# Kernel optimization log

Measured on AMD Instinct MI355X. Metric: run time of the kernel, lower is better.

## Reference

```python
import jax, jax.numpy as jnp
import numpy as np

NA, NT, E = 8000, 30000, 150000
H, C, HID = 4, 64, 64  # heads, per-head out_channels, hidden_dim
AF, TF = 32, 48


def _gat(x_src, x_dst, src, dst, W, a_src, a_dst, bias, n_dst):
    # PyG GATConv, concat=False, add_self_loops=False, eval (no dropout)
    h_src = (x_src @ W).reshape(-1, H, C)          # [Ns,H,C]
    h_dst = (x_dst @ W).reshape(-1, H, C)          # [Nd,H,C]
    al_s = jnp.sum(h_src * a_src, axis=-1)         # [Ns,H]
    al_d = jnp.sum(h_dst * a_dst, axis=-1)         # [Nd,H]
    e = jax.nn.leaky_relu(al_s[src] + al_d[dst], 0.2)  # [E,H]
    m = jax.ops.segment_max(e, dst, num_segments=n_dst)
    m = jnp.where(jnp.isfinite(m), m, 0.0)
    ex = jnp.exp(e - m[dst])
    den = jax.ops.segment_sum(ex, dst, num_segments=n_dst)
    alpha = ex / (den[dst] + 1e-16)                # per-dst softmax
    out = jax.ops.segment_sum(alpha[:, :, None] * h_src[src], dst, num_segments=n_dst)
    return jnp.mean(out, axis=1) + bias            # mean over heads + bias


def _bn(x, g, b):  # BatchNorm1d, training-mode batch stats, biased var
    mu = jnp.mean(x, axis=0)
    v = jnp.var(x, axis=0)
    return g * (x - mu) * jax.lax.rsqrt(v + 1e-5) + b


def _ln(x, g, b):
    mu = jnp.mean(x, axis=-1, keepdims=True)
    v = jnp.var(x, axis=-1, keepdims=True)
    return g * (x - mu) * jax.lax.rsqrt(v + 1e-5) + b


def setup_inputs() -> dict:
    key = jax.random.key(0)
    ks = jax.random.split(key, 40)
    n = lambda i, shp, s=0.05: jax.random.normal(ks[i], shp, jnp.float32) * s
    ri = lambda i, hi: jax.random.randint(ks[i], (E,), 0, hi, jnp.int32)
    inp = {
        'x_agent': jax.random.normal(ks[0], (NA, AF), jnp.float32),
        'x_track': jax.random.normal(ks[1], (NT, TF), jnp.float32),
        'ei_a2t1_src': ri(2, NA), 'ei_a2t1_dst': ri(3, NT),
        'ei_t2a1_src': ri(4, NT), 'ei_t2a1_dst': ri(5, NA),
        'ei_a2t2_src': ri(6, NA), 'ei_a2t2_dst': ri(7, NT),
        'ei_t2a2_src': ri(8, NT), 'ei_t2a2_dst': ri(9, NA),
        'ae_W': n(10, (AF, HID)), 'ae_b': jnp.zeros((HID,), jnp.float32),
        'te_W': n(11, (TF, HID)), 'te_b': jnp.zeros((HID,), jnp.float32),
        # stacked GATConv params: [layer=3, relation=4, ...]; rel order: a2t1,t2a1,a2t2,t2a2
        'conv_W': n(12, (3, 4, HID, H * C)),
        'conv_asrc': n(13, (3, 4, H, C)),
        'conv_adst': n(14, (3, 4, H, C)),
        'conv_bias': jnp.zeros((3, 4, C), jnp.float32),
        'bn_gamma': jnp.ones((3, 2, HID), jnp.float32),   # [layer, agent/track, HID]
        'bn_beta': jnp.zeros((3, 2, HID), jnp.float32),
        # actor heads: 0=agent_alpha,1=agent_beta,2=track_alpha,3=track_beta
        'actor_W1': n(15, (4, HID, HID // 2)), 'actor_b1': jnp.zeros((4, HID // 2), jnp.float32),
        'actor_g': jnp.ones((4, HID // 2), jnp.float32), 'actor_be': jnp.zeros((4, HID // 2), jnp.float32),
        'actor_W2': n(16, (4, HID // 2, 1)), 'actor_b2': jnp.zeros((4, 1), jnp.float32),
        # critic global value head
        'cW1': n(17, (HID * 6, HID * 2)), 'cb1': jnp.zeros((HID * 2,), jnp.float32),
        'cg1': jnp.ones((HID * 2,), jnp.float32), 'cbe1': jnp.zeros((HID * 2,), jnp.float32),
        'cW2': n(18, (HID * 2, HID)), 'cb2': jnp.zeros((HID,), jnp.float32),
        'cg2': jnp.ones((HID,), jnp.float32), 'cbe2': jnp.zeros((HID,), jnp.float32),
        'cW3': n(19, (HID, HID // 2)), 'cb3': jnp.zeros((HID // 2,), jnp.float32),
        'cW4': n(20, (HID // 2, 1)), 'cb4': jnp.zeros((1,), jnp.float32),
    }
    return inp


def _forward(x_agent, x_track,
             ei_a2t1_src, ei_a2t1_dst, ei_t2a1_src, ei_t2a1_dst,
             ei_a2t2_src, ei_a2t2_dst, ei_t2a2_src, ei_t2a2_dst,
             ae_W, ae_b, te_W, te_b,
             conv_W, conv_asrc, conv_adst, conv_bias,
             bn_gamma, bn_beta,
             actor_W1, actor_b1, actor_g, actor_be, actor_W2, actor_b2,
             cW1, cb1, cg1, cbe1, cW2, cb2, cg2, cbe2, cW3, cb3, cW4, cb4):
    xa = jax.nn.relu(x_agent @ ae_W + ae_b)
    xt = jax.nn.relu(x_track @ te_W + te_b)
    prev_a, prev_t = None, None
    for l in range(3):
        # HeteroConv aggr='mean': track <- mean(rel0, rel2); agent <- mean(rel1, rel3)
        ot = 0.5 * (_gat(xa, xt, ei_a2t1_src, ei_a2t1_dst, conv_W[l, 0], conv_asrc[l, 0], conv_adst[l, 0], conv_bias[l, 0], NT)
                    + _gat(xa, xt, ei_a2t2_src, ei_a2t2_dst, conv_W[l, 2], conv_asrc[l, 2], conv_adst[l, 2], conv_bias[l, 2], NT))
        oa = 0.5 * (_gat(xt, xa, ei_t2a1_src, ei_t2a1_dst, conv_W[l, 1], conv_asrc[l, 1], conv_adst[l, 1], conv_bias[l, 1], NA)
                    + _gat(xt, xa, ei_t2a2_src, ei_t2a2_dst, conv_W[l, 3], conv_asrc[l, 3], conv_adst[l, 3], conv_bias[l, 3], NA))
        oa = _bn(jax.nn.relu(oa), bn_gamma[l, 0], bn_beta[l, 0])
        ot = _bn(jax.nn.relu(ot), bn_gamma[l, 1], bn_beta[l, 1])
        if l > 0:  # residuals after layers 2 and 3
            oa = oa + prev_a
            ot = ot + prev_t
        prev_a, prev_t = oa, ot
        xa, xt = oa, ot

    def head(x, i):
        h = jax.nn.relu(_ln(x @ actor_W1[i] + actor_b1[i], actor_g[i], actor_be[i]))
        return jax.nn.softplus(h @ actor_W2[i] + actor_b2[i]) + 1.0

    aA, aB = head(xa, 0), head(xa, 1)
    tA, tB = head(xt, 2), head(xt, 3)
    aC = aA / (aA + aB)
    tC = tA / (tA + tB)

    # critic global value (torch.std is unbiased, ddof=1)
    g = jnp.concatenate([
        jnp.mean(xa, axis=0), jnp.max(xa, axis=0), jnp.std(xa, axis=0, ddof=1),
        jnp.mean(xt, axis=0), jnp.max(xt, axis=0), jnp.std(xt, axis=0, ddof=1)], axis=0)[None, :]
    h = jax.nn.relu(_ln(g @ cW1 + cb1, cg1, cbe1))
    h = jax.nn.relu(_ln(h @ cW2 + cb2, cg2, cbe2))
    h = jax.nn.relu(h @ cW3 + cb3)
    gv = jnp.squeeze(h @ cW4 + cb4)
    return aA, aB, aC, tA, tB, tC, gv


def reference(x_agent, x_track,
              ei_a2t1_src, ei_a2t1_dst, ei_t2a1_src, ei_t2a1_dst,
              ei_a2t2_src, ei_a2t2_dst, ei_t2a2_src, ei_t2a2_dst,
              ae_W, ae_b, te_W, te_b,
              conv_W, conv_asrc, conv_adst, conv_bias,
              bn_gamma, bn_beta,
              actor_W1, actor_b1, actor_g, actor_be, actor_W2, actor_b2,
              cW1, cb1, cg1, cbe1, cW2, cb2, cg2, cbe2, cW3, cb3, cW4, cb4):
    return _forward(x_agent, x_track,
                    ei_a2t1_src, ei_a2t1_dst, ei_t2a1_src, ei_t2a1_dst,
                    ei_a2t2_src, ei_a2t2_dst, ei_t2a2_src, ei_t2a2_dst,
                    ae_W, ae_b, te_W, te_b,
                    conv_W, conv_asrc, conv_adst, conv_bias,
                    bn_gamma, bn_beta,
                    actor_W1, actor_b1, actor_g, actor_be, actor_W2, actor_b2,
                    cW1, cb1, cg1, cbe1, cW2, cb2, cg2, cbe2, cW3, cb3, cW4, cb4)
```

## Files before the change

kernel.cpp:

```cpp
#include <hip/hip_runtime.h>
#include <math.h>

#define NAg 8000
#define NTr 30000
#define NE  150000

#define XA_OFF 0
#define XT_OFF 512000
#define H0_OFF 2432000
#define H1_OFF 4480000
#define H2_OFF 12160000
#define H3_OFF 14208000
#define BNSTB 8320000
#define ALS0 21888000
#define ALS1 21920000
#define ALS2 22040000
#define ALS3 22072000
#define ALD0 22192000
#define ALD1 22312000
#define ALD2 22344000
#define ALD3 22464000
#define ESRC_I 22496000
#define OAACC 23104000
#define OTACC 23616000
#define BNST 25536000
#define CST  25536256
#define ROWP_I 25536640
#define CURS_I 25656704
#define RELSTRIDE 30016

typedef unsigned short ushortT;

__device__ __forceinline__ float lrelu(float x){ return x >= 0.f ? x : 0.2f*x; }
__device__ __forceinline__ unsigned fmap(float f){ unsigned u=__float_as_uint(f); return (u&0x80000000u)? ~u : (u|0x80000000u); }
__device__ __forceinline__ float funmap(unsigned u){ return (u&0x80000000u)? __uint_as_float(u&0x7FFFFFFFu) : __uint_as_float(~u); }
__device__ __forceinline__ float softplusf(float x){ return fmaxf(x,0.f) + log1pf(expf(-fabsf(x))); }
__device__ __forceinline__ ushortT f2bf(float f){
  unsigned u = __float_as_uint(f);
  unsigned r = u + 0x7FFFu + ((u>>16)&1u);
  return (ushortT)(r>>16);
}
__device__ __forceinline__ float bf2f(ushortT s){ return __uint_as_float(((unsigned)s)<<16); }
__device__ __forceinline__ float wred32(float v){
  #pragma unroll
  for (int o=16;o;o>>=1) v += __shfl_xor(v,o,32);
  return v;
}
__device__ __forceinline__ int selH(int r){ return r==0?H0_OFF: r==1?H1_OFF: r==2?H2_OFF:H3_OFF; }
__device__ __forceinline__ int selALS(int r){ return r==0?ALS0: r==1?ALS1: r==2?ALS2:ALS3; }
__device__ __forceinline__ int selALD(int r){ return r==0?ALD0: r==1?ALD1: r==2?ALD2:ALD3; }

__global__ __launch_bounds__(256) void k_encoder(const float* xA, const float* xT,
    const float* aeW, const float* aeB, const float* teW, const float* teB, float* ws) {
  int type = blockIdx.y;
  int N = type ? NTr : NAg;
  int t = threadIdx.x, wv = t >> 6, lane = t & 63;
  int n = blockIdx.x*4 + wv;
  int F = type ? 48 : 32;
  const float* X = type ? xT : xA;
  const float* W = type ? teW : aeW;
  const float* B = type ? teB : aeB;
  float* out = ws + (type ? XT_OFF : XA_OFF);
  __shared__ float xs[4][48];
  if (n < N && lane < F) xs[wv][lane] = X[(size_t)n*F + lane];
  __syncthreads();
  if (n >= N) return;
  float acc = B[lane];
  for (int k = 0; k < F; ++k) acc += xs[wv][k] * W[k*64 + lane];
  out[(size_t)n*64 + lane] = fmaxf(acc, 0.f);
}

__global__ __launch_bounds__(256) void k_hist(const int* d0_,const int* d1_,const int* d2_,const int* d3_,
                                              int* wsi) {
  int r = blockIdx.y;
  const int* dp = r==0? d0_ : r==1? d1_ : r==2? d2_ : d3_;
  int e = blockIdx.x*256 + threadIdx.x;
  if (e >= NE) return;
  atomicAdd(&wsi[ROWP_I + r*RELSTRIDE + dp[e]], 1);
}

__global__ __launch_bounds__(256) void k_scan(int* wsi) {
  int r = blockIdx.x;
  int n = ((r & 1) ? NAg : NTr) + 1;
  int* rp = wsi + ROWP_I + r*RELSTRIDE;
  __shared__ int part[256];
  int t = threadIdx.x;
  int chunk = (n + 255) / 256;
  int lo = t*chunk, hi = min(lo + chunk, n);
  int s = 0;
  for (int i = lo; i < hi; ++i) s += rp[i];
  part[t] = s;
  __syncthreads();
  if (t == 0) {
    int run = 0;
    for (int i = 0; i < 256; ++i) { int tm = part[i]; part[i] = run; run += tm; }
  }
  __syncthreads();
  int run = part[t];
  for (int i = lo; i < hi; ++i) { int tm = rp[i]; rp[i] = run; run += tm; }
}

__global__ __launch_bounds__(256) void k_fill(const int* s0,const int* d0_,const int* s1,const int* d1_,
    const int* s2,const int* d2_,const int* s3,const int* d3_, int* wsi) {
  int r = blockIdx.y;
  const int* sp = r==0? s0 : r==1? s1 : r==2? s2 : s3;
  const int* dp = r==0? d0_ : r==1? d1_ : r==2? d2_ : d3_;
  int e = blockIdx.x*256 + threadIdx.x;
  if (e >= NE) return;
  int d = dp[e];
  int pos = wsi[ROWP_I + r*RELSTRIDE + d] + atomicAdd(&wsi[CURS_I + r*RELSTRIDE + d], 1);
  wsi[ESRC_I + r*NE + pos] = sp[e];
}

__global__ __launch_bounds__(256) void k_alx(const float* convW, const float* convAsrc,
                                             const float* convAdst, float* ws, int layer) {
  int y = blockIdx.y;
  int side = y >> 2;
  int r = y & 3;
  int Nn = side ? ((r & 1) ? NTr : NAg) : ((r & 1) ? NAg : NTr);
  if (blockIdx.x * 64 >= Nn) return;
  const float* W  = convW + (size_t)(layer*4 + r)*64*256;
  const float* av = (side ? convAsrc : convAdst) + (size_t)(layer*4 + r)*256;
  __shared__ float Wv[64*4];
  int t = threadIdx.x;
  {
    int k = t >> 2, h = t & 3;
    float s = 0.f;
    for (int c = 0; c < 64; ++c) s += W[k*256 + h*64 + c] * av[h*64 + c];
    Wv[k*4 + h] = s;
  }
  __syncthreads();
  const float* xv = ws + (side ? ((r & 1) ? XT_OFF : XA_OFF) : ((r & 1) ? XA_OFF : XT_OFF));
  float* outp = ws + (side ? selALS(r) : selALD(r));
  int n = blockIdx.x * 64 + (t >> 2);
  if (n >= Nn) return;
  int h = t & 3;
  float s = 0.f;
  for (int k = 0; k < 64; ++k) s += xv[(size_t)n*64 + k] * Wv[k*4 + h];
  outp[n*4 + h] = s;
}

__global__ __launch_bounds__(256) void k_hgemm(const float* convW, float* ws, int layer) {
  int tile = blockIdx.x;
  int r, row0;
  if (tile < 500)        { r = 0; row0 = tile*16; }
  else if (tile < 2375)  { r = 1; row0 = (tile-500)*16; }
  else if (tile < 2875)  { r = 2; row0 = (tile-2375)*16; }
  else                   { r = 3; row0 = (tile-2875)*16; }
  const float* W  = convW + (size_t)(layer*4 + r)*64*256;
  const float* xg = ws + ((r & 1) ? XT_OFF : XA_OFF);
  ushortT* h16 = (ushortT*)(ws + selH(r));
  __shared__ float xs[16][64];
  int t = threadIdx.x;
  #pragma unroll
  for (int i = 0; i < 4; ++i) {
    int lin = i*256 + t;
    xs[lin>>6][lin&63] = xg[((size_t)row0 + (lin>>6))*64 + (lin&63)];
  }
  __syncthreads();
  int c0 = t & 63;
  int tr = t >> 6;
  float acc[4][4];
  #pragma unroll
  for (int i=0;i<4;i++){ acc[i][0]=0;acc[i][1]=0;acc[i][2]=0;acc[i][3]=0; }
  const float* Wc = W + c0;
  for (int k4 = 0; k4 < 16; ++k4) {
    float4 xv[4];
    #pragma unroll
    for (int i = 0; i < 4; ++i) xv[i] = *(const float4*)&xs[tr*4+i][k4*4];
    #pragma unroll
    for (int kk = 0; kk < 4; ++kk) {
      int k = k4*4 + kk;
      float w0 = Wc[k*256], w1 = Wc[k*256+64], w2 = Wc[k*256+128], w3 = Wc[k*256+192];
      #pragma unroll
      for (int i = 0; i < 4; ++i) {
        float x = (kk==0)?xv[i].x:(kk==1)?xv[i].y:(kk==2)?xv[i].z:xv[i].w;
        acc[i][0] += x*w0; acc[i][1] += x*w1; acc[i][2] += x*w2; acc[i][3] += x*w3;
      }
    }
  }
  #pragma unroll
  for (int i = 0; i < 4; ++i) {
    int row = row0 + tr*4 + i;
    ushort4 pk;
    pk.x = f2bf(acc[i][0]); pk.y = f2bf(acc[i][1]);
    pk.z = f2bf(acc[i][2]); pk.w = f2bf(acc[i][3]);
    *(ushort4*)(h16 + (size_t)row*256 + c0*4) = pk;
  }
}

__global__ __launch_bounds__(256) void k_agg(const float* convBias, float* ws, int layer) {
  int type = blockIdx.y;
  int N = type ? NAg : NTr;
  if (blockIdx.x * 4 >= N) return;
  int t = threadIdx.x, lane = t & 63, hh = lane & 3, base = lane & ~3;
  int node = blockIdx.x*4 + (t >> 6);
  const int* wsi = (const int*)ws;
  float outv = 0.f;
  #pragma unroll
  for (int rr = 0; rr < 2; ++rr) {
    int r = type ? (rr ? 3 : 1) : (rr ? 2 : 0);
    const int* rp = wsi + ROWP_I + r*RELSTRIDE;
    const int* es = wsi + ESRC_I + r*NE;
    const float* als = ws + selALS(r);
    const ushortT* h16 = (const ushortT*)(ws + selH(r));
    float ad = (ws + selALD(r))[node*4 + hh];
    int p = rp[node], p1 = rp[node+1];
    float num0=0.f, num1=0.f, num2=0.f, num3=0.f, den=0.f;
    for (; p + 4 <= p1; p += 4) {
      int sa = es[p], sb = es[p+1], sc = es[p+2], sd4 = es[p+3];
      ushort4 va = *(const ushort4*)(h16 + (size_t)sa*256 + lane*4);
      ushort4 vb = *(const ushort4*)(h16 + (size_t)sb*256 + lane*4);
      ushort4 vc = *(const ushort4*)(h16 + (size_t)sc*256 + lane*4);
      ushort4 vd = *(const ushort4*)(h16 + (size_t)sd4*256 + lane*4);
      float la = als[sa*4+hh], lb = als[sb*4+hh], lc = als[sc*4+hh], ld = als[sd4*4+hh];
      float ea = __expf(lrelu(la + ad));
      float eb = __expf(lrelu(lb + ad));
      float ec = __expf(lrelu(lc + ad));
      float ed = __expf(lrelu(ld + ad));
      den += (ea+eb)+(ec+ed);
      float qa0=__shfl(ea,base), qa1=__shfl(ea,base+1), qa2=__shfl(ea,base+2), qa3=__shfl(ea,base+3);
      float qb0=__shfl(eb,base), qb1=__shfl(eb,base+1), qb2=__shfl(eb,base+2), qb3=__shfl(eb,base+3);
      float qc0=__shfl(ec,base), qc1=__shfl(ec,base+1), qc2=__shfl(ec,base+2), qc3=__shfl(ec,base+3);
      float qd0=__shfl(ed,base), qd1=__shfl(ed,base+1), qd2=__shfl(ed,base+2), qd3=__shfl(ed,base+3);
      num0 += qa0*bf2f(va.x) + qb0*bf2f(vb.x) + qc0*bf2f(vc.x) + qd0*bf2f(vd.x);
      num1 += qa1*bf2f(va.y) + qb1*bf2f(vb.y) + qc1*bf2f(vc.y) + qd1*bf2f(vd.y);
      num2 += qa2*bf2f(va.z) + qb2*bf2f(vb.z) + qc2*bf2f(vc.z) + qd2*bf2f(vd.z);
      num3 += qa3*bf2f(va.w) + qb3*bf2f(vb.w) + qc3*bf2f(vc.w) + qd3*bf2f(vd.w);
    }
    for (; p < p1; ++p) {
      int s = es[p];
      ushort4 va = *(const ushort4*)(h16 + (size_t)s*256 + lane*4);
      float e = __expf(lrelu(als[s*4 + hh] + ad));
      den += e;
      float q0 = __shfl(e, base), q1 = __shfl(e, base+1), q2 = __shfl(e, base+2), q3 = __shfl(e, base+3);
      num0 += q0*bf2f(va.x); num1 += q1*bf2f(va.y); num2 += q2*bf2f(va.z); num3 += q3*bf2f(va.w);
    }
    float rd = 1.f/(den + 1e-16f);
    float r0 = __shfl(rd, base), r1 = __shfl(rd, base+1), r2 = __shfl(rd, base+2), r3 = __shfl(rd, base+3);
    outv += num0*r0 + num1*r1 + num2*r2 + num3*r3;
  }
  int rA = type ? 1 : 0, rB = type ? 3 : 2;
  float bavg = 0.5f*(convBias[(layer*4 + rA)*64 + lane] + convBias[(layer*4 + rB)*64 + lane]);
  float z = fmaxf(outv*0.125f + bavg, 0.f);
  float* acc = ws + (type ? OAACC : OTACC);
  acc[(size_t)node*64 + lane] = z;
  __shared__ float sdm[2][256];
  sdm[0][t] = z; sdm[1][t] = z*z;
  __syncthreads();
  if (t < 64) {
    float s1 = sdm[0][t] + sdm[0][t+64] + sdm[0][t+128] + sdm[0][t+192];
    float s2 = sdm[1][t] + sdm[1][t+64] + sdm[1][t+128] + sdm[1][t+192];
    int bt = type ? 0 : 1;
    int bucket = blockIdx.x & 63;
    atomicAdd(&ws[BNSTB + bucket*256 + bt*128 + t], s1);
    atomicAdd(&ws[BNSTB + bucket*256 + bt*128 + 64 + t], s2);
  }
}

__global__ __launch_bounds__(256) void k_bnred(float* ws) {
  int t = threadIdx.x;
  float s = 0.f;
  #pragma unroll
  for (int b = 0; b < 64; ++b) s += ws[BNSTB + b*256 + t];
  ws[BNST + t] = s;
}

__global__ __launch_bounds__(256) void k_bnnorm(const float* bnG, const float* bnB, float* ws, int layer) {
  int type = blockIdx.y;
  int N = type ? NTr : NAg;
  float* acc = ws + (type ? OTACC : OAACC);
  float* x = ws + (type ? XT_OFF : XA_OFF);
  int i = blockIdx.x*256 + threadIdx.x;
  if (i >= N*64) return;
  int c = i & 63;
  float Nf = (float)N;
  float s1 = ws[BNST + type*128 + c], s2 = ws[BNST + type*128 + 64 + c];
  float mu = s1/Nf, var = s2/Nf - mu*mu;
  float g = bnG[(layer*2 + type)*64 + c], b = bnB[(layer*2 + type)*64 + c];
  float y = g*(acc[i]-mu)*rsqrtf(var + 1e-5f) + b;
  if (layer > 0) y += x[i];
  x[i] = y;
}

__global__ __launch_bounds__(256) void k_actor(const float* aW1, const float* ab1, const float* ag,
    const float* abe, const float* aW2, const float* ab2, const float* ws, float* out) {
  int type = blockIdx.y;
  int N = type ? NTr : NAg;
  int t = threadIdx.x, wv = t >> 6, lane = t & 63;
  int p = lane >> 5, j = lane & 31;
  int n = blockIdx.x*4 + wv;
  const float* xg = ws + (type ? XT_OFF : XA_OFF);
  __shared__ float xsh[4][64];
  {
    int nn = blockIdx.x*4 + (t >> 6);
    if (nn < N) xsh[t >> 6][t & 63] = xg[(size_t)nn*64 + (t & 63)];
  }
  __syncthreads();
  if (n >= N) return;
  int i = (type ? 2 : 0) + p;
  const float* W = aW1 + i*2048 + j;
  float a0 = 0.f, a1 = 0.f, a2 = 0.f, a3 = 0.f;
  #pragma unroll
  for (int k = 0; k < 64; k += 4) {
    a0 += xsh[wv][k]   * W[k*32];
    a1 += xsh[wv][k+1] * W[(k+1)*32];
    a2 += xsh[wv][k+2] * W[(k+2)*32];
    a3 += xsh[wv][k+3] * W[(k+3)*32];
  }
  float tv = ((a0+a1)+(a2+a3)) + ab1[i*32 + j];
  float mu = wred32(tv) * (1.f/32.f);
  float dz = tv - mu;
  float var = wred32(dz*dz) * (1.f/32.f);
  float hn = fmaxf(ag[i*32+j]*dz*rsqrtf(var + 1e-5f) + abe[i*32+j], 0.f);
  float s = wred32(hn * aW2[i*32 + j]) + ab2[i];
  float val = softplusf(s) + 1.f;
  float vA = __shfl(val, 0);
  float vB = __shfl(val, 32);
  if (lane == 0) {
    int offA = type ? 24000 : 0, offB = type ? 54000 : 8000, offC = type ? 84000 : 16000;
    out[offA + n] = vA;
    out[offB + n] = vB;
    out[offC + n] = vA / (vA + vB);
  }
}

__global__ __launch_bounds__(256) void k_criticstats(float* ws) {
  int type = blockIdx.y;
  int N = type ? NTr : NAg;
  const float* x = ws + (type ? XT_OFF : XA_OFF);
  int t = threadIdx.x;
  int c = t & 63;
  float s1 = 0.f, s2 = 0.f, mx = -3.4e38f;
  for (int n = blockIdx.x*4 + (t>>6); n < N; n += gridDim.x*4) {
    float v = x[(size_t)n*64 + c];
    s1 += v; s2 += v*v; mx = fmaxf(mx, v);
  }
  __shared__ float sd[3][256];
  sd[0][t]=s1; sd[1][t]=s2; sd[2][t]=mx;
  __syncthreads();
  if (t < 64) {
    s1 = sd[0][t]+sd[0][t+64]+sd[0][t+128]+sd[0][t+192];
    s2 = sd[1][t]+sd[1][t+64]+sd[1][t+128]+sd[1][t+192];
    mx = fmaxf(fmaxf(sd[2][t],sd[2][t+64]), fmaxf(sd[2][t+128],sd[2][t+192]));
    atomicAdd(&ws[CST + type*192 + c], s1);
    atomicAdd(&ws[CST + type*192 + 64 + c], s2);
    atomicMax((unsigned*)&ws[CST + type*192 + 128 + c], fmap(mx));
  }
}

__device__ __forceinline__ float blocksum128(float v, float* red) {
  int t = threadIdx.x;
  red[t] = v; __syncthreads();
  #pragma unroll
  for (int s = 64; s > 0; s >>= 1) { if (t < s) red[t] += red[t+s]; __syncthreads(); }
  float r = red[0]; __syncthreads();
  return r;
}

__global__ __launch_bounds__(128) void k_critic(const float* cW1,const float* cb1,const float* cg1,const float* cbe1,
    const float* cW2,const float* cb2,const float* cg2,const float* cbe2,
    const float* cW3,const float* cb3,const float* cW4,const float* cb4,
    const float* ws, float* out) {
  __shared__ float g[384];
  __shared__ float h1[128];
  __shared__ float h2s[64];
  __shared__ float red[128];
  int t = threadIdx.x;
  if (t < 64) {
    #pragma unroll
    for (int type = 0; type < 2; ++type) {
      float Nf = type ? 30000.f : 8000.f;
      float s1 = ws[CST + type*192 + t];
      float s2 = ws[CST + type*192 + 64 + t];
      unsigned mu_ = __float_as_uint(ws[CST + type*192 + 128 + t]);
      float mean = s1 / Nf;
      float sd = sqrtf(fmaxf((s2 - Nf*mean*mean) / (Nf - 1.f), 0.f));
      g[type*192 + t] = mean;
      g[type*192 + 64 + t] = funmap(mu_);
      g[type*192 + 128 + t] = sd;
    }
  }
  __syncthreads();
  float v = cb1[t];
  for (int k = 0; k < 384; ++k) v += g[k] * cW1[k*128 + t];
  float mu = blocksum128(v, red) * (1.f/128.f);
  float d = v - mu;
  float var = blocksum128(d*d, red) * (1.f/128.f);
  h1[t] = fmaxf(cg1[t]*d*rsqrtf(var + 1e-5f) + cbe1[t], 0.f);
  __syncthreads();
  float v2 = 0.f;
  if (t < 64) { v2 = cb2[t]; for (int k = 0; k < 128; ++k) v2 += h1[k] * cW2[k*64 + t]; }
  float mu2 = blocksum128(t < 64 ? v2 : 0.f, red) * (1.f/64.f);
  float d2 = v2 - mu2;
  float var2 = blocksum128(t < 64 ? d2*d2 : 0.f, red) * (1.f/64.f);
  if (t < 64) h2s[t] = fmaxf(cg2[t]*d2*rsqrtf(var2 + 1e-5f) + cbe2[t], 0.f);
  __syncthreads();
  float v3 = 0.f;
  if (t < 32) {
    v3 = cb3[t];
    for (int k = 0; k < 64; ++k) v3 += h2s[k] * cW3[k*32 + t];
    v3 = fmaxf(v3, 0.f);
  }
  float s4 = blocksum128(t < 32 ? v3 * cW4[t] : 0.f, red);
  if (t == 0) out[114000] = s4 + cb4[0];
}

extern "C" void kernel_launch(void* const* d_in, const int* in_sizes, int n_in,
                              void* d_out, int out_size, void* d_ws, size_t ws_size,
                              hipStream_t stream) {
  const float* x_agent = (const float*)d_in[0];
  const float* x_track = (const float*)d_in[1];
  const int* s0 = (const int*)d_in[2]; const int* d0_ = (const int*)d_in[3];
  const int* s1 = (const int*)d_in[4]; const int* d1_ = (const int*)d_in[5];
  const int* s2 = (const int*)d_in[6]; const int* d2_ = (const int*)d_in[7];
  const int* s3 = (const int*)d_in[8]; const int* d3_ = (const int*)d_in[9];
  const float* aeW = (const float*)d_in[10]; const float* aeB = (const float*)d_in[11];
  const float* teW = (const float*)d_in[12]; const float* teB = (const float*)d_in[13];
  const float* convW    = (const float*)d_in[14];
  const float* convAsrc = (const float*)d_in[15];
  const float* convAdst = (const float*)d_in[16];
  const float* convBias = (const float*)d_in[17];
  const float* bnG = (const float*)d_in[18]; const float* bnB = (const float*)d_in[19];
  const float* aW1 = (const float*)d_in[20]; const float* ab1 = (const float*)d_in[21];
  const float* ag  = (const float*)d_in[22]; const float* abe = (const float*)d_in[23];
  const float* aW2 = (const float*)d_in[24]; const float* ab2 = (const float*)d_in[25];
  const float* cW1 = (const float*)d_in[26]; const float* cb1 = (const float*)d_in[27];
  const float* cg1 = (const float*)d_in[28]; const float* cbe1 = (const float*)d_in[29];
  const float* cW2 = (const float*)d_in[30]; const float* cb2 = (const float*)d_in[31];
  const float* cg2 = (const float*)d_in[32]; const float* cbe2 = (const float*)d_in[33];
  const float* cW3 = (const float*)d_in[34]; const float* cb3 = (const float*)d_in[35];
  const float* cW4 = (const float*)d_in[36]; const float* cb4 = (const float*)d_in[37];
  float* ws = (float*)d_ws;
  int* wsi = (int*)d_ws;
  float* out = (float*)d_out;

  hipMemsetAsync(wsi + ROWP_I, 0, (size_t)240128 * sizeof(int), stream);
  hipMemsetAsync(ws + CST, 0, (size_t)384 * sizeof(float), stream);

  k_encoder<<<dim3(7500, 2), 256, 0, stream>>>(x_agent, x_track, aeW, aeB, teW, teB, ws);

  k_hist<<<dim3(586, 4), 256, 0, stream>>>(d0_, d1_, d2_, d3_, wsi);
  k_scan<<<dim3(4), 256, 0, stream>>>(wsi);
  k_fill<<<dim3(586, 4), 256, 0, stream>>>(s0,d0_,s1,d1_,s2,d2_,s3,d3_, wsi);

  for (int l = 0; l < 3; ++l) {
    hipMemsetAsync(ws + BNSTB, 0, (size_t)16384 * sizeof(float), stream);
    k_alx<<<dim3(469, 8), 256, 0, stream>>>(convW, convAsrc, convAdst, ws, l);
    k_hgemm<<<dim3(4750), 256, 0, stream>>>(convW, ws, l);
    k_agg<<<dim3(7500, 2), 256, 0, stream>>>(convBias, ws, l);
    k_bnred<<<1, 256, 0, stream>>>(ws);
    k_bnnorm<<<dim3(7500, 2), 256, 0, stream>>>(bnG, bnB, ws, l);
  }

  k_criticstats<<<dim3(128, 2), 256, 0, stream>>>(ws);
  k_actor<<<dim3(7500, 2), 256, 0, stream>>>(aW1, ab1, ag, abe, aW2, ab2, ws, out);
  k_critic<<<1, 128, 0, stream>>>(cW1,cb1,cg1,cbe1,cW2,cb2,cg2,cbe2,cW3,cb3,cW4,cb4, ws, out);
}
```

Measured before the change: 678.1 us.

## Rebalance GAT aggregation grid and stage node features in LDS for attention logits

The aggregation kernel moves from a 2D grid with many idle blocks to a flat 11500-block grid. Agent nodes, which have about 19 edges per relation, now get one wavefront per relation, two nodes per block, and the two partial results are combined through shared memory. Track nodes keep one wavefront per node covering both relations. Separately, the attention-logit kernel stages 64 rows of features in padded shared memory before the dot product, replacing strided per-thread global reads.

```diff
diff --git a/kernel.cpp b/kernel.cpp
--- a/kernel.cpp
+++ b/kernel.cpp
@@ -50,6 +50,43 @@
 __device__ __forceinline__ int selALS(int r){ return r==0?ALS0: r==1?ALS1: r==2?ALS2:ALS3; }
 __device__ __forceinline__ int selALD(int r){ return r==0?ALD0: r==1?ALD1: r==2?ALD2:ALD3; }
 
+__device__ __forceinline__ float agg_rel(const int* es, int p, int p1, const float* als,
+                                         const ushortT* h16, float ad, int lane, int hh, int base) {
+  float num0=0.f, num1=0.f, num2=0.f, num3=0.f, den=0.f;
+  for (; p + 4 <= p1; p += 4) {
+    int sa = es[p], sb = es[p+1], sc = es[p+2], sd4 = es[p+3];
+    ushort4 va = *(const ushort4*)(h16 + (size_t)sa*256 + lane*4);
+    ushort4 vb = *(const ushort4*)(h16 + (size_t)sb*256 + lane*4);
+    ushort4 vc = *(const ushort4*)(h16 + (size_t)sc*256 + lane*4);
+    ushort4 vd = *(const ushort4*)(h16 + (size_t)sd4*256 + lane*4);
+    float la = als[sa*4+hh], lb = als[sb*4+hh], lc = als[sc*4+hh], ld = als[sd4*4+hh];
+    float ea = __expf(lrelu(la + ad));
+    float eb = __expf(lrelu(lb + ad));
+    float ec = __expf(lrelu(lc + ad));
+    float ed = __expf(lrelu(ld + ad));
+    den += (ea+eb)+(ec+ed);
+    float qa0=__shfl(ea,base), qa1=__shfl(ea,base+1), qa2=__shfl(ea,base+2), qa3=__shfl(ea,base+3);
+    float qb0=__shfl(eb,base), qb1=__shfl(eb,base+1), qb2=__shfl(eb,base+2), qb3=__shfl(eb,base+3);
+    float qc0=__shfl(ec,base), qc1=__shfl(ec,base+1), qc2=__shfl(ec,base+2), qc3=__shfl(ec,base+3);
+    float qd0=__shfl(ed,base), qd1=__shfl(ed,base+1), qd2=__shfl(ed,base+2), qd3=__shfl(ed,base+3);
+    num0 += qa0*bf2f(va.x) + qb0*bf2f(vb.x) + qc0*bf2f(vc.x) + qd0*bf2f(vd.x);
+    num1 += qa1*bf2f(va.y) + qb1*bf2f(vb.y) + qc1*bf2f(vc.y) + qd1*bf2f(vd.y);
+    num2 += qa2*bf2f(va.z) + qb2*bf2f(vb.z) + qc2*bf2f(vc.z) + qd2*bf2f(vd.z);
+    num3 += qa3*bf2f(va.w) + qb3*bf2f(vb.w) + qc3*bf2f(vc.w) + qd3*bf2f(vd.w);
+  }
+  for (; p < p1; ++p) {
+    int s = es[p];
+    ushort4 va = *(const ushort4*)(h16 + (size_t)s*256 + lane*4);
+    float e = __expf(lrelu(als[s*4 + hh] + ad));
+    den += e;
+    float q0 = __shfl(e, base), q1 = __shfl(e, base+1), q2 = __shfl(e, base+2), q3 = __shfl(e, base+3);
+    num0 += q0*bf2f(va.x); num1 += q1*bf2f(va.y); num2 += q2*bf2f(va.z); num3 += q3*bf2f(va.w);
+  }
+  float rd = 1.f/(den + 1e-16f);
+  float r0 = __shfl(rd, base), r1 = __shfl(rd, base+1), r2 = __shfl(rd, base+2), r3 = __shfl(rd, base+3);
+  return num0*r0 + num1*r1 + num2*r2 + num3*r3;
+}
+
 __global__ __launch_bounds__(256) void k_encoder(const float* xA, const float* xT,
     const float* aeW, const float* aeB, const float* teW, const float* teB, float* ws) {
   int type = blockIdx.y;
@@ -118,10 +155,12 @@
   int side = y >> 2;
   int r = y & 3;
   int Nn = side ? ((r & 1) ? NTr : NAg) : ((r & 1) ? NAg : NTr);
-  if (blockIdx.x * 64 >= Nn) return;
+  int n0 = blockIdx.x * 64;
+  if (n0 >= Nn) return;
   const float* W  = convW + (size_t)(layer*4 + r)*64*256;
   const float* av = (side ? convAsrc : convAdst) + (size_t)(layer*4 + r)*256;
   __shared__ float Wv[64*4];
+  __shared__ float xsh[64][65];
   int t = threadIdx.x;
   {
     int k = t >> 2, h = t & 3;
@@ -129,15 +168,20 @@
     for (int c = 0; c < 64; ++c) s += W[k*256 + h*64 + c] * av[h*64 + c];
     Wv[k*4 + h] = s;
   }
-  __syncthreads();
   const float* xv = ws + (side ? ((r & 1) ? XT_OFF : XA_OFF) : ((r & 1) ? XA_OFF : XT_OFF));
-  float* outp = ws + (side ? selALS(r) : selALD(r));
-  int n = blockIdx.x * 64 + (t >> 2);
-  if (n >= Nn) return;
-  int h = t & 3;
+  #pragma unroll
+  for (int i = 0; i < 16; ++i) {
+    int lin = i*256 + t;
+    int nn = lin >> 6, k = lin & 63;
+    xsh[nn][k] = (n0 + nn < Nn) ? xv[((size_t)n0 + nn)*64 + k] : 0.f;
+  }
+  __syncthreads();
+  int n = t >> 2, h = t & 3;
+  if (n0 + n >= Nn) return;
   float s = 0.f;
-  for (int k = 0; k < 64; ++k) s += xv[(size_t)n*64 + k] * Wv[k*4 + h];
-  outp[n*4 + h] = s;
+  #pragma unroll
+  for (int k = 0; k < 64; ++k) s += xsh[n][k] * Wv[k*4 + h];
+  (ws + (side ? selALS(r) : selALD(r)))[(size_t)(n0 + n)*4 + h] = s;
 }
 
 __global__ __launch_bounds__(256) void k_hgemm(const float* convW, float* ws, int layer) {
@@ -190,71 +234,65 @@
 }
 
 __global__ __launch_bounds__(256) void k_agg(const float* convBias, float* ws, int layer) {
-  int type = blockIdx.y;
-  int N = type ? NAg : NTr;
-  if (blockIdx.x * 4 >= N) return;
-  int t = threadIdx.x, lane = t & 63, hh = lane & 3, base = lane & ~3;
-  int node = blockIdx.x*4 + (t >> 6);
+  int t = threadIdx.x, wv = t >> 6, lane = t & 63, hh = lane & 3, base = lane & ~3;
   const int* wsi = (const int*)ws;
-  float outv = 0.f;
-  #pragma unroll
-  for (int rr = 0; rr < 2; ++rr) {
-    int r = type ? (rr ? 3 : 1) : (rr ? 2 : 0);
+  int bid = blockIdx.x;
+  __shared__ float part[4][64];
+  __shared__ float sh1[4][64];
+  __shared__ float sh2[4][64];
+  if (bid < 4000) {
+    int node = bid*2 + (wv >> 1);
+    int rr = wv & 1;
+    int r = rr ? 3 : 1;
     const int* rp = wsi + ROWP_I + r*RELSTRIDE;
     const int* es = wsi + ESRC_I + r*NE;
     const float* als = ws + selALS(r);
     const ushortT* h16 = (const ushortT*)(ws + selH(r));
     float ad = (ws + selALD(r))[node*4 + hh];
-    int p = rp[node], p1 = rp[node+1];
-    float num0=0.f, num1=0.f, num2=0.f, num3=0.f, den=0.f;
-    for (; p + 4 <= p1; p += 4) {
-      int sa = es[p], sb = es[p+1], sc = es[p+2], sd4 = es[p+3];
-      ushort4 va = *(const ushort4*)(h16 + (size_t)sa*256 + lane*4);
-      ushort4 vb = *(const ushort4*)(h16 + (size_t)sb*256 + lane*4);
-      ushort4 vc = *(const ushort4*)(h16 + (size_t)sc*256 + lane*4);
-      ushort4 vd = *(const ushort4*)(h16 + (size_t)sd4*256 + lane*4);
-      float la = als[sa*4+hh], lb = als[sb*4+hh], lc = als[sc*4+hh], ld = als[sd4*4+hh];
-      float ea = __expf(lrelu(la + ad));
-      float eb = __expf(lrelu(lb + ad));
-      float ec = __expf(lrelu(lc + ad));
-      float ed = __expf(lrelu(ld + ad));
-      den += (ea+eb)+(ec+ed);
-      float qa0=__shfl(ea,base), qa1=__shfl(ea,base+1), qa2=__shfl(ea,base+2), qa3=__shfl(ea,base+3);
-      float qb0=__shfl(eb,base), qb1=__shfl(eb,base+1), qb2=__shfl(eb,base+2), qb3=__shfl(eb,base+3);
-      float qc0=__shfl(ec,base), qc1=__shfl(ec,base+1), qc2=__shfl(ec,base+2), qc3=__shfl(ec,base+3);
-      float qd0=__shfl(ed,base), qd1=__shfl(ed,base+1), qd2=__shfl(ed,base+2), qd3=__shfl(ed,base+3);
-      num0 += qa0*bf2f(va.x) + qb0*bf2f(vb.x) + qc0*bf2f(vc.x) + qd0*bf2f(vd.x);
-      num1 += qa1*bf2f(va.y) + qb1*bf2f(vb.y) + qc1*bf2f(vc.y) + qd1*bf2f(vd.y);
-      num2 += qa2*bf2f(va.z) + qb2*bf2f(vb.z) + qc2*bf2f(vc.z) + qd2*bf2f(vd.z);
-      num3 += qa3*bf2f(va.w) + qb3*bf2f(vb.w) + qc3*bf2f(vc.w) + qd3*bf2f(vd.w);
-    }
-    for (; p < p1; ++p) {
-      int s = es[p];
-      ushort4 va = *(const ushort4*)(h16 + (size_t)s*256 + lane*4);
-      float e = __expf(lrelu(als[s*4 + hh] + ad));
-      den += e;
-      float q0 = __shfl(e, base), q1 = __shfl(e, base+1), q2 = __shfl(e, base+2), q3 = __shfl(e, base+3);
-      num0 += q0*bf2f(va.x); num1 += q1*bf2f(va.y); num2 += q2*bf2f(va.z); num3 += q3*bf2f(va.w);
-    }
-    float rd = 1.f/(den + 1e-16f);
-    float r0 = __shfl(rd, base), r1 = __shfl(rd, base+1), r2 = __shfl(rd, base+2), r3 = __shfl(rd, base+3);
-    outv += num0*r0 + num1*r1 + num2*r2 + num3*r3;
-  }
-  int rA = type ? 1 : 0, rB = type ? 3 : 2;
-  float bavg = 0.5f*(convBias[(layer*4 + rA)*64 + lane] + convBias[(layer*4 + rB)*64 + lane]);
-  float z = fmaxf(outv*0.125f + bavg, 0.f);
-  float* acc = ws + (type ? OAACC : OTACC);
-  acc[(size_t)node*64 + lane] = z;
-  __shared__ float sdm[2][256];
-  sdm[0][t] = z; sdm[1][t] = z*z;
-  __syncthreads();
-  if (t < 64) {
-    float s1 = sdm[0][t] + sdm[0][t+64] + sdm[0][t+128] + sdm[0][t+192];
-    float s2 = sdm[1][t] + sdm[1][t+64] + sdm[1][t+128] + sdm[1][t+192];
-    int bt = type ? 0 : 1;
-    int bucket = blockIdx.x & 63;
-    atomicAdd(&ws[BNSTB + bucket*256 + bt*128 + t], s1);
-    atomicAdd(&ws[BNSTB + bucket*256 + bt*128 + 64 + t], s2);
+    part[wv][lane] = agg_rel(es, rp[node], rp[node+1], als, h16, ad, lane, hh, base);
+    __syncthreads();
+    if (rr == 0) {
+      float o = part[wv][lane] + part[wv+1][lane];
+      float bavg = 0.5f*(convBias[(layer*4 + 1)*64 + lane] + convBias[(layer*4 + 3)*64 + lane]);
+      float z = fmaxf(o*0.125f + bavg, 0.f);
+      ws[OAACC + (size_t)node*64 + lane] = z;
+      sh1[wv][lane] = z; sh2[wv][lane] = z*z;
+    } else {
+      sh1[wv][lane] = 0.f; sh2[wv][lane] = 0.f;
+    }
+    __syncthreads();
+    if (t < 64) {
+      float s1 = sh1[0][t] + sh1[1][t] + sh1[2][t] + sh1[3][t];
+      float s2 = sh2[0][t] + sh2[1][t] + sh2[2][t] + sh2[3][t];
+      int bucket = bid & 63;
+      atomicAdd(&ws[BNSTB + bucket*256 + t], s1);
+      atomicAdd(&ws[BNSTB + bucket*256 + 64 + t], s2);
+    }
+  } else {
+    int node = (bid - 4000)*4 + wv;
+    float outv = 0.f;
+    #pragma unroll
+    for (int rr = 0; rr < 2; ++rr) {
+      int r = rr ? 2 : 0;
+      const int* rp = wsi + ROWP_I + r*RELSTRIDE;
+      const int* es = wsi + ESRC_I + r*NE;
+      const float* als = ws + selALS(r);
+      const ushortT* h16 = (const ushortT*)(ws + selH(r));
+      float ad = (ws + selALD(r))[node*4 + hh];
+      outv += agg_rel(es, rp[node], rp[node+1], als, h16, ad, lane, hh, base);
+    }
+    float bavg = 0.5f*(convBias[(layer*4 + 0)*64 + lane] + convBias[(layer*4 + 2)*64 + lane]);
+    float z = fmaxf(outv*0.125f + bavg, 0.f);
+    ws[OTACC + (size_t)node*64 + lane] = z;
+    sh1[wv][lane] = z; sh2[wv][lane] = z*z;
+    __syncthreads();
+    if (t < 64) {
+      float s1 = sh1[0][t] + sh1[1][t] + sh1[2][t] + sh1[3][t];
+      float s2 = sh2[0][t] + sh2[1][t] + sh2[2][t] + sh2[3][t];
+      int bucket = bid & 63;
+      atomicAdd(&ws[BNSTB + bucket*256 + 128 + t], s1);
+      atomicAdd(&ws[BNSTB + bucket*256 + 192 + t], s2);
+    }
   }
 }
 
@@ -448,7 +486,7 @@
     hipMemsetAsync(ws + BNSTB, 0, (size_t)16384 * sizeof(float), stream);
     k_alx<<<dim3(469, 8), 256, 0, stream>>>(convW, convAsrc, convAdst, ws, l);
     k_hgemm<<<dim3(4750), 256, 0, stream>>>(convW, ws, l);
-    k_agg<<<dim3(7500, 2), 256, 0, stream>>>(convBias, ws, l);
+    k_agg<<<dim3(11500), 256, 0, stream>>>(convBias, ws, l);
     k_bnred<<<1, 256, 0, stream>>>(ws);
     k_bnnorm<<<dim3(7500, 2), 256, 0, stream>>>(bnG, bnB, ws, l);
   }
```

Result: slower. 724.8 us (+6.9%).
